# Performance work log

Hardware: AMD Instinct MI355X
Metric: run time of the kernel (lower is better)

The kernel has to match this reference:

```python
import jax, jax.numpy as jnp
import numpy as np

B_, DIM, NPTS = 16, 128, 16384
J, K, L = 16, 128, 128   # kernel_mode, GkNN_mode_out, GkNN_mode_in
R, M1, M2 = 8, 64, 64    # low-rank A/B dims and mask modes


def setup_inputs() -> dict:
    key = jax.random.key(0)
    ks = jax.random.split(key, 9)
    scale = 1.0 / (L * K)
    return {
        "x": jax.random.normal(ks[0], (B_, DIM, NPTS), jnp.float32),
        "bases": jax.random.normal(ks[1], (NPTS, K), jnp.float32),
        "wbases": jax.random.normal(ks[2], (NPTS, L), jnp.float32),
        "product": jax.random.normal(ks[3], (K, L), jnp.float32),
        "D_out": jax.random.normal(ks[4], (J, K), jnp.float32),
        "D_in": jax.random.normal(ks[5], (J, L), jnp.float32),
        "A": jax.random.normal(ks[6], (J, R, M1), jnp.float32),
        "B": jax.random.normal(ks[7], (J, R, M2), jnp.float32),
        "weights": scale * jax.random.normal(ks[8], (DIM, DIM, J), jnp.float32),
    }


def reference(x, bases, wbases, product, D_out, D_in, A, B, weights):
    # project onto weighted bases: (b, c, npts) @ (npts, L) -> (b, c, L)
    x_hat = jnp.einsum('bcx,xl->bcl', x, wbases)
    # H tensor: (J, K, L) broadcast product + low-rank correction
    H = D_out[:, :, None] * D_in[:, None, :] * product[None, :, :]
    Q = jnp.einsum('jrm,jrn->jmn', A, B)  # bmm(A^T, B): (J, M1, M2)
    H = H.at[:, :Q.shape[1], :Q.shape[2]].add(Q)
    # mode mixing: (J,K,L) x (b,i,L) -> (b,i,J,K), then weights (i,o,J)
    x_hat1 = jnp.einsum('jkl,bil->bijk', H, x_hat)
    y = jnp.einsum('ioj,bijk->bok', weights, x_hat1)
    # back to physical space: (b, o, K) x (npts, K) -> (b, o, npts)
    return jnp.einsum('bok,xk->box', y, bases)
```

## Files before the change

### kernel.cpp

```cpp
#include <hip/hip_runtime.h>

#define B_    16
#define DIM   128
#define NPTS  16384
#define J_    16
#define K_    128
#define L_    128
#define R_    8
#define M1_   64

typedef float  f32x4 __attribute__((ext_vector_type(4)));
typedef short  s16x8 __attribute__((ext_vector_type(8)));
typedef unsigned short u16;
typedef u16 u16x8 __attribute__((ext_vector_type(8)));
typedef u16 u16x4 __attribute__((ext_vector_type(4)));

__device__ __forceinline__ u16 f2bf(float f) {
    unsigned u = __float_as_uint(f);
    u += 0x7FFFu + ((u >> 16) & 1u);
    return (u16)(u >> 16);
}
#define MFMA16(a,b,c) __builtin_amdgcn_mfma_f32_16x16x32_bf16((a),(b),(c),0,0,0)

#define OFF_PARTA 0u
#define OFF_WBT   8388608u
#define OFF_BASB  12582912u
#define OFF_HKL   16777216u
#define OFF_W2T   17301504u
#define OFF_XHB   17825792u
#define OFF_YB    18350080u
#define OFF_YP    18874368u

__global__ __launch_bounds__(256) void k_prep(
    const float* __restrict__ product, const float* __restrict__ Do,
    const float* __restrict__ Di, const float* __restrict__ A,
    const float* __restrict__ Bm, const float* __restrict__ W,
    const float* __restrict__ wb, const float* __restrict__ bases,
    u16* __restrict__ Hkl, u16* __restrict__ W2T,
    u16* __restrict__ wbT, u16* __restrict__ basesb)
{
    __shared__ u16 sT[128][136];
    const int bid = blockIdx.x, t = threadIdx.x;
    if (bid < 1024) {
        int idx = (bid << 8) | t;
        int j = idx >> 14, k = (idx >> 7) & 127, l = idx & 127;
        float v = Do[j*K_ + k] * Di[j*L_ + l] * product[k*L_ + l];
        if (k < M1_ && l < M1_) {
            float q = 0.f;
            #pragma unroll
            for (int r = 0; r < R_; ++r)
                q += A[(j*R_ + r)*M1_ + k] * Bm[(j*R_ + r)*M1_ + l];
            v += q;
        }
        Hkl[idx] = f2bf(v);
    } else if (bid < 2048) {
        int idx = ((bid - 1024) << 8) | t;
        int o = idx >> 11, ji = idx & 2047, j = ji >> 7, i = ji & 127;
        W2T[idx] = f2bf(W[(i*DIM + o)*J_ + j]);
    } else if (bid < 2176) {
        const int p0 = (bid - 2048) * 128;
        #pragma unroll
        for (int it = 0; it < 16; ++it) {
            int idx = it*256 + t, row = idx >> 5, c4 = (idx & 31) * 4;
            float4 v = *(const float4*)(wb + (size_t)(p0+row)*L_ + c4);
            sT[c4+0][row] = f2bf(v.x); sT[c4+1][row] = f2bf(v.y);
            sT[c4+2][row] = f2bf(v.z); sT[c4+3][row] = f2bf(v.w);
        }
        __syncthreads();
        #pragma unroll
        for (int it = 0; it < 8; ++it) {
            int idx = it*256 + t, l = idx >> 4, pc = (idx & 15) * 8;
            *(u16x8*)(wbT + (size_t)l*NPTS + p0 + pc) = *(const u16x8*)&sT[l][pc];
        }
    } else {
        int i = (((bid - 2176) << 8) | t) * 4;
        float4 v = *(const float4*)(bases + i);
        u16x4 o4 = { f2bf(v.x), f2bf(v.y), f2bf(v.z), f2bf(v.w) };
        *(u16x4*)(basesb + i) = o4;
    }
}

__global__ __launch_bounds__(512) void k_stageA(
    const float* __restrict__ x, const u16* __restrict__ wbT,
    float* __restrict__ part)
{
    __shared__ u16 sA[2][64][136];
    __shared__ u16 sB[2][128][136];
    const int t = threadIdx.x, lane = t & 63, wave = t >> 6;
    const int quad = lane >> 4, l16 = lane & 15;
    const int wr = wave >> 2, wc = wave & 3;
    const int m0 = blockIdx.x * 64;
    const size_t pbase = (size_t)blockIdx.y * 2048;

    f32x4 acc[2][2] = {};
    const int ac4 = (t & 31) * 4, arr = t >> 5;
    const int bc8 = (t & 15) * 8, brr = t >> 4;

    #pragma unroll
    for (int i = 0; i < 4; ++i) {
        int row = arr + 16*i;
        float4 v = *(const float4*)(x + (size_t)(m0+row)*NPTS + pbase + ac4);
        u16x4 h = { f2bf(v.x), f2bf(v.y), f2bf(v.z), f2bf(v.w) };
        *(u16x4*)&sA[0][row][ac4] = h;
    }
    #pragma unroll
    for (int i = 0; i < 4; ++i) {
        int row = brr + 32*i;
        *(u16x8*)&sB[0][row][bc8] =
            *(const u16x8*)(wbT + (size_t)row*NPTS + pbase + bc8);
    }

    int cur = 0;
    for (int c = 0; c < 16; ++c) {
        __syncthreads();
        float4 vx[4]; u16x8 vb[4];
        if (c < 15) {
            const size_t pb = pbase + (size_t)(c+1)*128;
            #pragma unroll
            for (int i = 0; i < 4; ++i)
                vx[i] = *(const float4*)(x + (size_t)(m0+arr+16*i)*NPTS + pb + ac4);
            #pragma unroll
            for (int i = 0; i < 4; ++i)
                vb[i] = *(const u16x8*)(wbT + (size_t)(brr+32*i)*NPTS + pb + bc8);
        }
        #pragma unroll
        for (int ks = 0; ks < 4; ++ks) {
            int kb = ks*32 + quad*8;
            s16x8 a0 = *(const s16x8*)&sA[cur][wr*32      + l16][kb];
            s16x8 a1 = *(const s16x8*)&sA[cur][wr*32 + 16 + l16][kb];
            s16x8 b0 = *(const s16x8*)&sB[cur][wc*32      + l16][kb];
            s16x8 b1 = *(const s16x8*)&sB[cur][wc*32 + 16 + l16][kb];
            acc[0][0] = MFMA16(a0, b0, acc[0][0]);
            acc[0][1] = MFMA16(a0, b1, acc[0][1]);
            acc[1][0] = MFMA16(a1, b0, acc[1][0]);
            acc[1][1] = MFMA16(a1, b1, acc[1][1]);
        }
        if (c < 15) {
            int nxt = cur ^ 1;
            #pragma unroll
            for (int i = 0; i < 4; ++i) {
                u16x4 h = { f2bf(vx[i].x), f2bf(vx[i].y), f2bf(vx[i].z), f2bf(vx[i].w) };
                *(u16x4*)&sA[nxt][arr+16*i][ac4] = h;
            }
            #pragma unroll
            for (int i = 0; i < 4; ++i)
                *(u16x8*)&sB[nxt][brr+32*i][bc8] = vb[i];
        }
        cur ^= 1;
    }

    float* po = part + (size_t)blockIdx.y * (2048*128);
    #pragma unroll
    for (int mt = 0; mt < 2; ++mt)
      #pragma unroll
      for (int r = 0; r < 4; ++r) {
        int row = m0 + wr*32 + mt*16 + quad*4 + r;
        #pragma unroll
        for (int nt = 0; nt < 2; ++nt) {
            int col = wc*32 + nt*16 + l16;
            po[(size_t)row*128 + col] = acc[mt][nt][r];
        }
      }
}

__global__ __launch_bounds__(256) void k_reduceA(
    const float* __restrict__ part, u16* __restrict__ xhatb)
{
    const float4* p4 = (const float4*)part;
    int i = blockIdx.x * 256 + threadIdx.x;
    float4 s = {0.f, 0.f, 0.f, 0.f};
    #pragma unroll
    for (int p = 0; p < 8; ++p) {
        float4 v = p4[(size_t)p*65536 + i];
        s.x += v.x; s.y += v.y; s.z += v.z; s.w += v.w;
    }
    u16x4 o4 = { f2bf(s.x), f2bf(s.y), f2bf(s.z), f2bf(s.w) };
    *(u16x4*)(xhatb + (size_t)i*4) = o4;
}

__global__ __launch_bounds__(256) void k_mix1(
    const u16* __restrict__ Hkl, const u16* __restrict__ xhatb,
    u16* __restrict__ Tt)
{
    __shared__ u16 sA[64][136];
    __shared__ u16 sB[128][136];
    const int t = threadIdx.x, lane = t & 63, wave = t >> 6;
    const int quad = lane >> 4, l16 = lane & 15;
    const int wr = wave >> 1, wc = wave & 1;
    const int b = blockIdx.x, j = blockIdx.y, kh = blockIdx.z;
    const u16* ha = Hkl + j*16384 + kh*64*128;
    const u16* xb = xhatb + b*16384;

    const int c8 = (t & 15)*8, rr = t >> 4;
    #pragma unroll
    for (int i = 0; i < 4; ++i) {
        int row = rr + 16*i;
        *(u16x8*)&sA[row][c8] = *(const u16x8*)(ha + row*128 + c8);
    }
    #pragma unroll
    for (int i = 0; i < 8; ++i) {
        int row = rr + 16*i;
        *(u16x8*)&sB[row][c8] = *(const u16x8*)(xb + row*128 + c8);
    }
    __syncthreads();

    f32x4 acc[2][4] = {};
    #pragma unroll
    for (int ks = 0; ks < 4; ++ks) {
        int kb = ks*32 + quad*8;
        s16x8 a[2], bf[4];
        #pragma unroll
        for (int mt = 0; mt < 2; ++mt) a[mt]  = *(const s16x8*)&sA[wr*32 + mt*16 + l16][kb];
        #pragma unroll
        for (int nt = 0; nt < 4; ++nt) bf[nt] = *(const s16x8*)&sB[wc*64 + nt*16 + l16][kb];
        #pragma unroll
        for (int mt = 0; mt < 2; ++mt)
            #pragma unroll
            for (int nt = 0; nt < 4; ++nt)
                acc[mt][nt] = MFMA16(a[mt], bf[nt], acc[mt][nt]);
    }
    u16* to = Tt + (size_t)b*262144 + (j << 7);
    #pragma unroll
    for (int mt = 0; mt < 2; ++mt)
      #pragma unroll
      for (int r = 0; r < 4; ++r) {
        int k = kh*64 + wr*32 + mt*16 + quad*4 + r;
        #pragma unroll
        for (int nt = 0; nt < 4; ++nt) {
            int i = wc*64 + nt*16 + l16;
            to[(size_t)k*2048 + i] = f2bf(acc[mt][nt][r]);
        }
      }
}

__global__ __launch_bounds__(256) void k_mix2(
    const u16* __restrict__ W2T, const u16* __restrict__ Tt,
    float* __restrict__ ypart)
{
    __shared__ u16 sA[64][136];
    __shared__ u16 sB[128][136];
    const int t = threadIdx.x, lane = t & 63, wave = t >> 6;
    const int quad = lane >> 4, l16 = lane & 15;
    const int wr = wave >> 1, wc = wave & 1;
    const int b = blockIdx.x, c = blockIdx.y, oh = blockIdx.z;
    const int ji0 = c * 128;
    const u16* tb = Tt + (size_t)b*262144;

    const int c8 = (t & 15)*8, rr = t >> 4;
    #pragma unroll
    for (int i = 0; i < 4; ++i) {
        int row = rr + 16*i;
        *(u16x8*)&sA[row][c8] = *(const u16x8*)(W2T + (size_t)(oh*64+row)*2048 + ji0 + c8);
    }
    #pragma unroll
    for (int i = 0; i < 8; ++i) {
        int row = rr + 16*i;
        *(u16x8*)&sB[row][c8] = *(const u16x8*)(tb + (size_t)row*2048 + ji0 + c8);
    }
    __syncthreads();

    f32x4 acc[2][4] = {};
    #pragma unroll
    for (int ks = 0; ks < 4; ++ks) {
        int kb = ks*32 + quad*8;
        s16x8 a[2], bf[4];
        #pragma unroll
        for (int mt = 0; mt < 2; ++mt) a[mt]  = *(const s16x8*)&sA[wr*32 + mt*16 + l16][kb];
        #pragma unroll
        for (int nt = 0; nt < 4; ++nt) bf[nt] = *(const s16x8*)&sB[wc*64 + nt*16 + l16][kb];
        #pragma unroll
        for (int mt = 0; mt < 2; ++mt)
            #pragma unroll
            for (int nt = 0; nt < 4; ++nt)
                acc[mt][nt] = MFMA16(a[mt], bf[nt], acc[mt][nt]);
    }
    float* yo = ypart + ((size_t)(c*16 + b) << 14);
    #pragma unroll
    for (int mt = 0; mt < 2; ++mt)
      #pragma unroll
      for (int r = 0; r < 4; ++r) {
        int o = oh*64 + wr*32 + mt*16 + quad*4 + r;
        #pragma unroll
        for (int nt = 0; nt < 4; ++nt) {
            int k = wc*64 + nt*16 + l16;
            yo[(size_t)o*128 + k] = acc[mt][nt][r];
        }
      }
}

__global__ __launch_bounds__(256) void k_reduceY(
    const float* __restrict__ part, u16* __restrict__ yb)
{
    const float4* p4 = (const float4*)part;
    int i = blockIdx.x * 256 + threadIdx.x;
    float4 s = {0.f, 0.f, 0.f, 0.f};
    #pragma unroll
    for (int p = 0; p < 16; ++p) {
        float4 v = p4[(size_t)p*65536 + i];
        s.x += v.x; s.y += v.y; s.z += v.z; s.w += v.w;
    }
    u16x4 o4 = { f2bf(s.x), f2bf(s.y), f2bf(s.z), f2bf(s.w) };
    *(u16x4*)(yb + (size_t)i*4) = o4;
}

__global__ __launch_bounds__(256) void k_stageE(
    const u16* __restrict__ yb, const u16* __restrict__ basesb,
    float* __restrict__ out)
{
    __shared__ u16 sA[128][136];
    __shared__ u16 sB[128][136];
    const int t = threadIdx.x, lane = t & 63, wave = t >> 6;
    const int quad = lane >> 4, l16 = lane & 15;
    const int wr = wave >> 1, wc = wave & 1;
    const int bo0 = blockIdx.x * 128, p0 = blockIdx.y * 128;

    const int c8 = (t & 15)*8, rr = t >> 4;
    #pragma unroll
    for (int i = 0; i < 8; ++i) {
        int row = rr + 16*i;
        *(u16x8*)&sA[row][c8] = *(const u16x8*)(yb     + (size_t)(bo0+row)*128 + c8);
        *(u16x8*)&sB[row][c8] = *(const u16x8*)(basesb + (size_t)(p0 +row)*128 + c8);
    }
    __syncthreads();

    f32x4 acc[4][4] = {};
    #pragma unroll
    for (int ks = 0; ks < 4; ++ks) {
        int kb = ks*32 + quad*8;
        s16x8 a[4], bf[4];
        #pragma unroll
        for (int mt = 0; mt < 4; ++mt) a[mt]  = *(const s16x8*)&sA[wr*64 + mt*16 + l16][kb];
        #pragma unroll
        for (int nt = 0; nt < 4; ++nt) bf[nt] = *(const s16x8*)&sB[wc*64 + nt*16 + l16][kb];
        #pragma unroll
        for (int mt = 0; mt < 4; ++mt)
            #pragma unroll
            for (int nt = 0; nt < 4; ++nt)
                acc[mt][nt] = MFMA16(a[mt], bf[nt], acc[mt][nt]);
    }
    #pragma unroll
    for (int mt = 0; mt < 4; ++mt)
      #pragma unroll
      for (int r = 0; r < 4; ++r) {
        size_t row = bo0 + wr*64 + mt*16 + quad*4 + r;
        #pragma unroll
        for (int nt = 0; nt < 4; ++nt) {
            int p = p0 + wc*64 + nt*16 + l16;
            out[row*NPTS + p] = acc[mt][nt][r];
        }
      }
}

extern "C" void kernel_launch(void* const* d_in, const int* in_sizes, int n_in,
                              void* d_out, int out_size, void* d_ws, size_t ws_size,
                              hipStream_t stream) {
    (void)in_sizes; (void)n_in; (void)out_size; (void)ws_size;
    const float* x       = (const float*)d_in[0];
    const float* bases   = (const float*)d_in[1];
    const float* wbases  = (const float*)d_in[2];
    const float* product = (const float*)d_in[3];
    const float* Do      = (const float*)d_in[4];
    const float* Di      = (const float*)d_in[5];
    const float* A       = (const float*)d_in[6];
    const float* Bm      = (const float*)d_in[7];
    const float* W       = (const float*)d_in[8];

    char* ws = (char*)d_ws;
    float* partA  = (float*)(ws + OFF_PARTA);
    u16*   Tt     = (u16*)  (ws + OFF_PARTA);
    u16*   wbT    = (u16*)  (ws + OFF_WBT);
    u16*   basesb = (u16*)  (ws + OFF_BASB);
    u16*   Hkl    = (u16*)  (ws + OFF_HKL);
    u16*   W2T    = (u16*)  (ws + OFF_W2T);
    u16*   xhatb  = (u16*)  (ws + OFF_XHB);
    u16*   yb     = (u16*)  (ws + OFF_YB);
    float* ypart  = (float*)(ws + OFF_YP);

    k_prep   <<<4224, 256, 0, stream>>>(product, Do, Di, A, Bm, W, wbases, bases,
                                        Hkl, W2T, wbT, basesb);
    k_stageA <<<dim3(32, 8), 512, 0, stream>>>(x, wbT, partA);
    k_reduceA<<<256, 256, 0, stream>>>(partA, xhatb);
    k_mix1   <<<dim3(16, 16, 2), 256, 0, stream>>>(Hkl, xhatb, Tt);
    k_mix2   <<<dim3(16, 16, 2), 256, 0, stream>>>(W2T, Tt, ypart);
    k_reduceY<<<256, 256, 0, stream>>>(ypart, yb);
    k_stageE <<<dim3(16, 128), 256, 0, stream>>>(yb, basesb, (float*)d_out);
}
```

Measured before the change: 318.4 us.

## Fuse mode-mixing GEMMs into one kernel and single-buffer stage A

Replaces the two mode-mixing GEMM kernels and the fp32 Y partial-sum reduction with one kernel. For each (batch, k-quarter, o-quarter) block it loops over j, computes the H·x_hat tile into shared memory, and accumulates W·T in registers, so the intermediate T and the Y partials never go to global memory. Stage A also drops its LDS double buffer for a single buffer with an extra barrier, which lowers shared-memory use but serialises the LDS refill against compute. The fused kernel recomputes H·x_hat for each o-quarter, launches only 256 blocks, and runs a serial j loop with two barriers per step.

Result: faster. 311.6 us, median of 2 (-2.1%).

```diff
diff --git a/kernel.cpp b/kernel.cpp
--- a/kernel.cpp
+++ b/kernel.cpp
@@ -29,7 +29,6 @@
 #define OFF_W2T   17301504u
 #define OFF_XHB   17825792u
 #define OFF_YB    18350080u
-#define OFF_YP    18874368u
 
 __global__ __launch_bounds__(256) void k_prep(
     const float* __restrict__ product, const float* __restrict__ Do,
@@ -84,8 +83,8 @@
     const float* __restrict__ x, const u16* __restrict__ wbT,
     float* __restrict__ part)
 {
-    __shared__ u16 sA[2][64][136];
-    __shared__ u16 sB[2][128][136];
+    __shared__ u16 sA[64][136];
+    __shared__ u16 sB[128][136];
     const int t = threadIdx.x, lane = t & 63, wave = t >> 6;
     const int quad = lane >> 4, l16 = lane & 15;
     const int wr = wave >> 2, wc = wave & 3;
@@ -96,24 +95,24 @@
     const int ac4 = (t & 31) * 4, arr = t >> 5;
     const int bc8 = (t & 15) * 8, brr = t >> 4;
 
+    float4 vx[4]; u16x8 vb[4];
+    #pragma unroll
+    for (int i = 0; i < 4; ++i)
+        vx[i] = *(const float4*)(x + (size_t)(m0+arr+16*i)*NPTS + pbase + ac4);
+    #pragma unroll
+    for (int i = 0; i < 4; ++i)
+        vb[i] = *(const u16x8*)(wbT + (size_t)(brr+32*i)*NPTS + pbase + bc8);
     #pragma unroll
     for (int i = 0; i < 4; ++i) {
-        int row = arr + 16*i;
-        float4 v = *(const float4*)(x + (size_t)(m0+row)*NPTS + pbase + ac4);
-        u16x4 h = { f2bf(v.x), f2bf(v.y), f2bf(v.z), f2bf(v.w) };
-        *(u16x4*)&sA[0][row][ac4] = h;
-    }
-    #pragma unroll
-    for (int i = 0; i < 4; ++i) {
-        int row = brr + 32*i;
-        *(u16x8*)&sB[0][row][bc8] =
-            *(const u16x8*)(wbT + (size_t)row*NPTS + pbase + bc8);
-    }
-
-    int cur = 0;
+        u16x4 h = { f2bf(vx[i].x), f2bf(vx[i].y), f2bf(vx[i].z), f2bf(vx[i].w) };
+        *(u16x4*)&sA[arr+16*i][ac4] = h;
+    }
+    #pragma unroll
+    for (int i = 0; i < 4; ++i)
+        *(u16x8*)&sB[brr+32*i][bc8] = vb[i];
+
     for (int c = 0; c < 16; ++c) {
         __syncthreads();
-        float4 vx[4]; u16x8 vb[4];
         if (c < 15) {
             const size_t pb = pbase + (size_t)(c+1)*128;
             #pragma unroll
@@ -126,27 +125,26 @@
         #pragma unroll
         for (int ks = 0; ks < 4; ++ks) {
             int kb = ks*32 + quad*8;
-            s16x8 a0 = *(const s16x8*)&sA[cur][wr*32      + l16][kb];
-            s16x8 a1 = *(const s16x8*)&sA[cur][wr*32 + 16 + l16][kb];
-            s16x8 b0 = *(const s16x8*)&sB[cur][wc*32      + l16][kb];
-            s16x8 b1 = *(const s16x8*)&sB[cur][wc*32 + 16 + l16][kb];
+            s16x8 a0 = *(const s16x8*)&sA[wr*32      + l16][kb];
+            s16x8 a1 = *(const s16x8*)&sA[wr*32 + 16 + l16][kb];
+            s16x8 b0 = *(const s16x8*)&sB[wc*32      + l16][kb];
+            s16x8 b1 = *(const s16x8*)&sB[wc*32 + 16 + l16][kb];
             acc[0][0] = MFMA16(a0, b0, acc[0][0]);
             acc[0][1] = MFMA16(a0, b1, acc[0][1]);
             acc[1][0] = MFMA16(a1, b0, acc[1][0]);
             acc[1][1] = MFMA16(a1, b1, acc[1][1]);
         }
+        __syncthreads();
         if (c < 15) {
-            int nxt = cur ^ 1;
             #pragma unroll
             for (int i = 0; i < 4; ++i) {
                 u16x4 h = { f2bf(vx[i].x), f2bf(vx[i].y), f2bf(vx[i].z), f2bf(vx[i].w) };
-                *(u16x4*)&sA[nxt][arr+16*i][ac4] = h;
+                *(u16x4*)&sA[arr+16*i][ac4] = h;
             }
             #pragma unroll
             for (int i = 0; i < 4; ++i)
-                *(u16x8*)&sB[nxt][brr+32*i][bc8] = vb[i];
-        }
-        cur ^= 1;
+                *(u16x8*)&sB[brr+32*i][bc8] = vb[i];
+        }
     }
 
     float* po = part + (size_t)blockIdx.y * (2048*128);
@@ -178,129 +176,89 @@
     *(u16x4*)(xhatb + (size_t)i*4) = o4;
 }
 
-__global__ __launch_bounds__(256) void k_mix1(
-    const u16* __restrict__ Hkl, const u16* __restrict__ xhatb,
-    u16* __restrict__ Tt)
-{
-    __shared__ u16 sA[64][136];
-    __shared__ u16 sB[128][136];
+__global__ __launch_bounds__(256) void k_mix(
+    const u16* __restrict__ Hkl, const u16* __restrict__ W2T,
+    const u16* __restrict__ xhatb, u16* __restrict__ yb)
+{
+    __shared__ u16 sXh[128][136];
+    __shared__ u16 sH[2][32][136];
+    __shared__ u16 sW[2][32][136];
+    __shared__ u16 sT[32][136];
     const int t = threadIdx.x, lane = t & 63, wave = t >> 6;
     const int quad = lane >> 4, l16 = lane & 15;
     const int wr = wave >> 1, wc = wave & 1;
-    const int b = blockIdx.x, j = blockIdx.y, kh = blockIdx.z;
-    const u16* ha = Hkl + j*16384 + kh*64*128;
-    const u16* xb = xhatb + b*16384;
-
-    const int c8 = (t & 15)*8, rr = t >> 4;
-    #pragma unroll
-    for (int i = 0; i < 4; ++i) {
-        int row = rr + 16*i;
-        *(u16x8*)&sA[row][c8] = *(const u16x8*)(ha + row*128 + c8);
-    }
+    const int b = blockIdx.x, kq = blockIdx.y, oq = blockIdx.z;
+
+    const int c8 = (t & 15) * 8, rr = t >> 4;
     #pragma unroll
     for (int i = 0; i < 8; ++i) {
         int row = rr + 16*i;
-        *(u16x8*)&sB[row][c8] = *(const u16x8*)(xb + row*128 + c8);
-    }
-    __syncthreads();
-
-    f32x4 acc[2][4] = {};
-    #pragma unroll
-    for (int ks = 0; ks < 4; ++ks) {
-        int kb = ks*32 + quad*8;
-        s16x8 a[2], bf[4];
-        #pragma unroll
-        for (int mt = 0; mt < 2; ++mt) a[mt]  = *(const s16x8*)&sA[wr*32 + mt*16 + l16][kb];
-        #pragma unroll
-        for (int nt = 0; nt < 4; ++nt) bf[nt] = *(const s16x8*)&sB[wc*64 + nt*16 + l16][kb];
-        #pragma unroll
-        for (int mt = 0; mt < 2; ++mt)
-            #pragma unroll
-            for (int nt = 0; nt < 4; ++nt)
-                acc[mt][nt] = MFMA16(a[mt], bf[nt], acc[mt][nt]);
-    }
-    u16* to = Tt + (size_t)b*262144 + (j << 7);
-    #pragma unroll
-    for (int mt = 0; mt < 2; ++mt)
-      #pragma unroll
-      for (int r = 0; r < 4; ++r) {
-        int k = kh*64 + wr*32 + mt*16 + quad*4 + r;
-        #pragma unroll
-        for (int nt = 0; nt < 4; ++nt) {
-            int i = wc*64 + nt*16 + l16;
-            to[(size_t)k*2048 + i] = f2bf(acc[mt][nt][r]);
-        }
-      }
-}
-
-__global__ __launch_bounds__(256) void k_mix2(
-    const u16* __restrict__ W2T, const u16* __restrict__ Tt,
-    float* __restrict__ ypart)
-{
-    __shared__ u16 sA[64][136];
-    __shared__ u16 sB[128][136];
-    const int t = threadIdx.x, lane = t & 63, wave = t >> 6;
-    const int quad = lane >> 4, l16 = lane & 15;
-    const int wr = wave >> 1, wc = wave & 1;
-    const int b = blockIdx.x, c = blockIdx.y, oh = blockIdx.z;
-    const int ji0 = c * 128;
-    const u16* tb = Tt + (size_t)b*262144;
-
-    const int c8 = (t & 15)*8, rr = t >> 4;
-    #pragma unroll
-    for (int i = 0; i < 4; ++i) {
+        *(u16x8*)&sXh[row][c8] =
+            *(const u16x8*)(xhatb + (size_t)b*16384 + row*128 + c8);
+    }
+    #pragma unroll
+    for (int i = 0; i < 2; ++i) {
         int row = rr + 16*i;
-        *(u16x8*)&sA[row][c8] = *(const u16x8*)(W2T + (size_t)(oh*64+row)*2048 + ji0 + c8);
-    }
-    #pragma unroll
-    for (int i = 0; i < 8; ++i) {
-        int row = rr + 16*i;
-        *(u16x8*)&sB[row][c8] = *(const u16x8*)(tb + (size_t)row*2048 + ji0 + c8);
-    }
-    __syncthreads();
-
-    f32x4 acc[2][4] = {};
-    #pragma unroll
-    for (int ks = 0; ks < 4; ++ks) {
-        int kb = ks*32 + quad*8;
-        s16x8 a[2], bf[4];
-        #pragma unroll
-        for (int mt = 0; mt < 2; ++mt) a[mt]  = *(const s16x8*)&sA[wr*32 + mt*16 + l16][kb];
-        #pragma unroll
-        for (int nt = 0; nt < 4; ++nt) bf[nt] = *(const s16x8*)&sB[wc*64 + nt*16 + l16][kb];
-        #pragma unroll
-        for (int mt = 0; mt < 2; ++mt)
-            #pragma unroll
-            for (int nt = 0; nt < 4; ++nt)
-                acc[mt][nt] = MFMA16(a[mt], bf[nt], acc[mt][nt]);
-    }
-    float* yo = ypart + ((size_t)(c*16 + b) << 14);
-    #pragma unroll
-    for (int mt = 0; mt < 2; ++mt)
-      #pragma unroll
-      for (int r = 0; r < 4; ++r) {
-        int o = oh*64 + wr*32 + mt*16 + quad*4 + r;
-        #pragma unroll
-        for (int nt = 0; nt < 4; ++nt) {
-            int k = wc*64 + nt*16 + l16;
-            yo[(size_t)o*128 + k] = acc[mt][nt][r];
-        }
-      }
-}
-
-__global__ __launch_bounds__(256) void k_reduceY(
-    const float* __restrict__ part, u16* __restrict__ yb)
-{
-    const float4* p4 = (const float4*)part;
-    int i = blockIdx.x * 256 + threadIdx.x;
-    float4 s = {0.f, 0.f, 0.f, 0.f};
-    #pragma unroll
-    for (int p = 0; p < 16; ++p) {
-        float4 v = p4[(size_t)p*65536 + i];
-        s.x += v.x; s.y += v.y; s.z += v.z; s.w += v.w;
-    }
-    u16x4 o4 = { f2bf(s.x), f2bf(s.y), f2bf(s.z), f2bf(s.w) };
-    *(u16x4*)(yb + (size_t)i*4) = o4;
+        *(u16x8*)&sH[0][row][c8] =
+            *(const u16x8*)(Hkl + (size_t)(kq*32 + row)*128 + c8);
+        *(u16x8*)&sW[0][row][c8] =
+            *(const u16x8*)(W2T + (size_t)(oq*32 + row)*2048 + c8);
+    }
+
+    f32x4 acc2 = {};
+    for (int j = 0; j < 16; ++j) {
+        const int cur = j & 1, nxt = cur ^ 1;
+        __syncthreads();
+        f32x4 acc1[4] = {};
+        #pragma unroll
+        for (int ks = 0; ks < 4; ++ks) {
+            int kb = ks*32 + quad*8;
+            s16x8 a = *(const s16x8*)&sH[cur][wr*16 + l16][kb];
+            #pragma unroll
+            for (int nt = 0; nt < 4; ++nt) {
+                s16x8 bf = *(const s16x8*)&sXh[wc*64 + nt*16 + l16][kb];
+                acc1[nt] = MFMA16(a, bf, acc1[nt]);
+            }
+        }
+        u16x8 hv[2], wv[2];
+        if (j < 15) {
+            #pragma unroll
+            for (int i = 0; i < 2; ++i) {
+                int row = rr + 16*i;
+                hv[i] = *(const u16x8*)(Hkl +
+                        ((size_t)(j+1)*128 + kq*32 + row)*128 + c8);
+                wv[i] = *(const u16x8*)(W2T +
+                        (size_t)(oq*32 + row)*2048 + (j+1)*128 + c8);
+            }
+        }
+        #pragma unroll
+        for (int nt = 0; nt < 4; ++nt)
+            #pragma unroll
+            for (int r = 0; r < 4; ++r)
+                sT[wr*16 + quad*4 + r][wc*64 + nt*16 + l16] = f2bf(acc1[nt][r]);
+        __syncthreads();
+        if (j < 15) {
+            #pragma unroll
+            for (int i = 0; i < 2; ++i) {
+                int row = rr + 16*i;
+                *(u16x8*)&sH[nxt][row][c8] = hv[i];
+                *(u16x8*)&sW[nxt][row][c8] = wv[i];
+            }
+        }
+        #pragma unroll
+        for (int ks = 0; ks < 4; ++ks) {
+            int kb = ks*32 + quad*8;
+            s16x8 a2 = *(const s16x8*)&sW[cur][wr*16 + l16][kb];
+            s16x8 b2 = *(const s16x8*)&sT[wc*16 + l16][kb];
+            acc2 = MFMA16(a2, b2, acc2);
+        }
+    }
+    #pragma unroll
+    for (int r = 0; r < 4; ++r) {
+        int o = oq*32 + wr*16 + quad*4 + r;
+        int k = kq*32 + wc*16 + l16;
+        yb[((size_t)b*128 + o)*128 + k] = f2bf(acc2[r]);
+    }
 }
 
 __global__ __launch_bounds__(256) void k_stageE(
@@ -367,21 +325,17 @@
 
     char* ws = (char*)d_ws;
     float* partA  = (float*)(ws + OFF_PARTA);
-    u16*   Tt     = (u16*)  (ws + OFF_PARTA);
     u16*   wbT    = (u16*)  (ws + OFF_WBT);
     u16*   basesb = (u16*)  (ws + OFF_BASB);
     u16*   Hkl    = (u16*)  (ws + OFF_HKL);
     u16*   W2T    = (u16*)  (ws + OFF_W2T);
     u16*   xhatb  = (u16*)  (ws + OFF_XHB);
     u16*   yb     = (u16*)  (ws + OFF_YB);
-    float* ypart  = (float*)(ws + OFF_YP);
 
     k_prep   <<<4224, 256, 0, stream>>>(product, Do, Di, A, Bm, W, wbases, bases,
                                         Hkl, W2T, wbT, basesb);
     k_stageA <<<dim3(32, 8), 512, 0, stream>>>(x, wbT, partA);
     k_reduceA<<<256, 256, 0, stream>>>(partA, xhatb);
-    k_mix1   <<<dim3(16, 16, 2), 256, 0, stream>>>(Hkl, xhatb, Tt);
-    k_mix2   <<<dim3(16, 16, 2), 256, 0, stream>>>(W2T, Tt, ypart);
-    k_reduceY<<<256, 256, 0, stream>>>(ypart, yb);
+    k_mix    <<<dim3(16, 4, 4), 256, 0, stream>>>(Hkl, W2T, xhatb, yb);
     k_stageE <<<dim3(16, 128), 256, 0, stream>>>(yb, basesb, (float*)d_out);
 }
```
